# Optimization experiments

Hardware: AMD Instinct MI355X
Metric: run time of the kernel (lower is better)

The kernel has to match this reference:

```python
import jax, jax.numpy as jnp
import numpy as np

D_MODEL = 1024
D_EXPERT = 1024
NUM_EXPERTS = 8
TOP_K = 2


def setup_inputs() -> dict:
    key = jax.random.key(0)
    k_x, k_r, k1, k2, k3 = jax.random.split(key, 5)
    scale = 0.02
    x = jax.random.normal(k_x, (4, 2048, D_MODEL), dtype=jnp.float32)
    Wr = jax.random.normal(k_r, (D_MODEL, NUM_EXPERTS), dtype=jnp.float32) * scale
    # stacked per-expert SwiGLU weights (Linear with bias=False)
    W1 = jax.random.normal(k1, (NUM_EXPERTS, D_MODEL, D_EXPERT), dtype=jnp.float32) * scale
    W2 = jax.random.normal(k2, (NUM_EXPERTS, D_EXPERT, D_MODEL), dtype=jnp.float32) * scale
    W3 = jax.random.normal(k3, (NUM_EXPERTS, D_MODEL, D_EXPERT), dtype=jnp.float32) * scale
    return {"x": x, "Wr": Wr, "W1": W1, "W2": W2, "W3": W3}


def reference(x, Wr, W1, W2, W3):
    B, T, C = x.shape
    xf = x.reshape(-1, C)                       # [N, C], N = B*T
    logits = xf @ Wr                            # [N, E]
    probs = jax.nn.softmax(logits, axis=-1)
    topk_p, topk_i = jax.lax.top_k(probs, TOP_K)  # [N, K]
    topk_p = topk_p / jnp.sum(topk_p, axis=-1, keepdims=True)
    out = jnp.zeros_like(xf)
    for e in range(NUM_EXPERTS):
        # combine weight per token for this expert (0 if not routed here)
        w_e = jnp.sum(topk_p * (topk_i == e), axis=-1)  # [N]
        h = jax.nn.silu(xf @ W1[e]) * (xf @ W3[e])       # [N, d_expert]
        y = h @ W2[e]                                    # [N, C]
        out = out + w_e[:, None] * y
    return out.reshape(B, T, C)
```

## Files before the change

kernel.cpp:

```cpp
#include <hip/hip_runtime.h>
#include <hip/hip_bf16.h>

typedef __attribute__((ext_vector_type(8))) short short8;
typedef __attribute__((ext_vector_type(4))) short short4v;
typedef __attribute__((ext_vector_type(4))) unsigned short ushort4v;
typedef __attribute__((ext_vector_type(4))) float f32x4;

#define NTOK 8192
#define DM 1024
#define DE 1024
#define NE 8

__device__ __forceinline__ float bf2f(unsigned short u) {
  union { unsigned int i; float f; } v; v.i = ((unsigned int)u) << 16; return v.f;
}
__device__ __forceinline__ unsigned short f2bf(float f) {
  union { float f; unsigned int i; } v; v.f = f;
  unsigned int lsb = (v.i >> 16) & 1;
  v.i += 0x7fffu + lsb;
  return (unsigned short)(v.i >> 16);
}
__device__ __forceinline__ void gl_lds(const short* g, short* l) {
  __builtin_amdgcn_global_load_lds((const __attribute__((address_space(1))) void*)g,
                                   (__attribute__((address_space(3))) void*)l, 16, 0, 0);
}

__global__ __launch_bounds__(256) void k_transw(const float* __restrict__ W1,
                                                const float* __restrict__ W2,
                                                const float* __restrict__ W3,
                                                short* __restrict__ wcat,
                                                short* __restrict__ w2t) {
  __shared__ float t[64][65];
  int mid = blockIdx.z;
  const float* src;
  if (mid < 8)       src = W1 + (size_t)mid * (DM * DE);
  else if (mid < 16) src = W3 + (size_t)(mid - 8) * (DM * DE);
  else               src = W2 + (size_t)(mid - 16) * (DE * DM);
  int tid = threadIdx.x;
  int tr = tid >> 4, tc = tid & 15;
  int kbase = blockIdx.y * 64, nbase = blockIdx.x * 64;
#pragma unroll
  for (int j = 0; j < 4; j++) {
    int kr = tr + j * 16;
    f32x4 v = *(const f32x4*)(src + (size_t)(kbase + kr) * 1024 + nbase + tc * 4);
    t[kr][tc * 4 + 0] = v[0]; t[kr][tc * 4 + 1] = v[1];
    t[kr][tc * 4 + 2] = v[2]; t[kr][tc * 4 + 3] = v[3];
  }
  __syncthreads();
#pragma unroll
  for (int j = 0; j < 4; j++) {
    int n = tr + j * 16;
    int ng = nbase + n;
    short4v o;
    o[0] = (short)f2bf(t[tc * 4 + 0][n]);
    o[1] = (short)f2bf(t[tc * 4 + 1][n]);
    o[2] = (short)f2bf(t[tc * 4 + 2][n]);
    o[3] = (short)f2bf(t[tc * 4 + 3][n]);
    size_t dsto;
    if (mid < 16) {
      int e = mid & 7, p = mid >> 3;
      int row_out = ((ng >> 6) * 128) + p * 64 + (ng & 63);
      dsto = (size_t)e * (2048 * 1024) + (size_t)row_out * 1024 + kbase + tc * 4;
      *(short4v*)(wcat + dsto) = o;
    } else {
      int e = mid - 16;
      dsto = (size_t)e * (1024 * 1024) + (size_t)ng * 1024 + kbase + tc * 4;
      *(short4v*)(w2t + dsto) = o;
    }
  }
}

__global__ __launch_bounds__(256) void k_router(const float* __restrict__ x,
                                                const float* __restrict__ Wr,
                                                short* __restrict__ xb,
                                                int* __restrict__ esel,
                                                float* __restrict__ wgt) {
  int wid = threadIdx.x >> 6, lane = threadIdx.x & 63;
  int t = blockIdx.x * 4 + wid;
  const float* xr = x + (size_t)t * DM;
  float acc[8];
#pragma unroll
  for (int e = 0; e < 8; e++) acc[e] = 0.f;
#pragma unroll
  for (int i = 0; i < 4; i++) {
    int kb = (i * 64 + lane) * 4;
    f32x4 v = *(const f32x4*)(xr + kb);
    ushort4v ob;
#pragma unroll
    for (int j = 0; j < 4; j++) {
      f32x4 w0 = *(const f32x4*)(Wr + (size_t)(kb + j) * 8);
      f32x4 w1 = *(const f32x4*)(Wr + (size_t)(kb + j) * 8 + 4);
      float xv = v[j];
      ob[j] = f2bf(xv);
      acc[0] += xv * w0[0]; acc[1] += xv * w0[1];
      acc[2] += xv * w0[2]; acc[3] += xv * w0[3];
      acc[4] += xv * w1[0]; acc[5] += xv * w1[1];
      acc[6] += xv * w1[2]; acc[7] += xv * w1[3];
    }
    *(ushort4v*)(xb + (size_t)t * DM + kb) = ob;
  }
#pragma unroll
  for (int off = 32; off; off >>= 1)
#pragma unroll
    for (int e = 0; e < 8; e++) acc[e] += __shfl_xor(acc[e], off);
  float m0 = -1e30f, m1 = -1e30f; int e0 = 0, e1 = 0;
#pragma unroll
  for (int e = 0; e < 8; e++) {
    float v = acc[e];
    if (v > m0) { m1 = m0; e1 = e0; m0 = v; e0 = e; }
    else if (v > m1) { m1 = v; e1 = e; }
  }
  float p = __expf(m1 - m0);
  if (lane == 0) {
    esel[2 * t] = e0; esel[2 * t + 1] = e1;
    wgt[2 * t] = 1.f / (1.f + p); wgt[2 * t + 1] = p / (1.f + p);
  }
}

__global__ __launch_bounds__(256) void k_rank(const int* __restrict__ esel,
                                              int* __restrict__ cnt,
                                              int* __restrict__ rank) {
  __shared__ int wcnt[4][8];
  __shared__ int woff[4][8];
  int tid = threadIdx.x;
  int lane = tid & 63, wid = tid >> 6;
  int t = blockIdx.x * 256 + tid;
  int e0 = esel[2 * t], e1 = esel[2 * t + 1];
  unsigned long long lt = (lane == 0) ? 0ull : ((~0ull) >> (64 - lane));
  int r0 = 0, r1 = 0;
#pragma unroll
  for (int e = 0; e < 8; e++) {
    unsigned long long m0 = __ballot(e0 == e);
    unsigned long long m1 = __ballot(e1 == e);
    int c0 = __popcll(m0);
    if (e0 == e) r0 = __popcll(m0 & lt);
    if (e1 == e) r1 = c0 + __popcll(m1 & lt);
    if (lane == 0) wcnt[wid][e] = c0 + __popcll(m1);
  }
  __syncthreads();
  if (tid < 8) {
    int e = tid;
    int c0 = wcnt[0][e], c1 = wcnt[1][e], c2 = wcnt[2][e], c3 = wcnt[3][e];
    int base = atomicAdd(&cnt[e], c0 + c1 + c2 + c3);
    woff[0][e] = base;
    woff[1][e] = base + c0;
    woff[2][e] = base + c0 + c1;
    woff[3][e] = base + c0 + c1 + c2;
  }
  __syncthreads();
  rank[2 * t] = woff[wid][e0] + r0;
  rank[2 * t + 1] = woff[wid][e1] + r1;
}

__global__ void k_offsets(const int* __restrict__ cnt, int* __restrict__ off) {
  if (threadIdx.x == 0) {
    int s = 0;
    for (int e = 0; e < NE; e++) { off[e] = s; s += cnt[e]; }
  }
}

__global__ __launch_bounds__(256) void k_scatter(const int* __restrict__ off,
                                                 const int* __restrict__ esel,
                                                 const int* __restrict__ rank,
                                                 int* __restrict__ tok_of_slot,
                                                 int* __restrict__ slot_of_tok) {
  int t = blockIdx.x * 256 + threadIdx.x;
#pragma unroll
  for (int j = 0; j < 2; j++) {
    int e = esel[2 * t + j];
    int s = off[e] + rank[2 * t + j];
    tok_of_slot[s] = t;
    slot_of_tok[2 * t + j] = s;
  }
}

template<int FFN1>
__global__ __launch_bounds__(512, 4) void k_ffn(const short* __restrict__ Abase,
                                                const short* __restrict__ Bbase,
                                                const int* __restrict__ cnt,
                                                const int* __restrict__ off,
                                                const int* __restrict__ tok_of_slot,
                                                short* __restrict__ outp) {
  const int e = blockIdx.y;
  const int cnt_e = cnt[e];
  const int m0 = blockIdx.z * 256;
  if (m0 >= cnt_e) return;
  const int bse = off[e];
  const int n0 = blockIdx.x * 128;
  const short* Bt = Bbase + (size_t)e * ((FFN1 ? 2048 : 1024) * 1024) + (size_t)n0 * 1024;

  __shared__ __align__(128) short Al[3][8192];
  __shared__ __align__(128) short Bl[3][4096];

  const int tid = threadIdx.x;
  const int lane = tid & 63, wid = tid >> 6;
  const int wr = wid >> 1, wcn = wid & 1;

  const short* srcA0; const short* srcA1; const short* srcB0;
  {
    int r0 = tid >> 2, c0 = (tid & 3) ^ ((r0 >> 1) & 3);
    int row0 = m0 + r0; if (row0 >= cnt_e) row0 = cnt_e - 1;
    long ar0 = FFN1 ? (long)tok_of_slot[bse + row0] : (long)(bse + row0);
    srcA0 = Abase + ar0 * 1024 + c0 * 8;
    int ch1 = tid + 512;
    int r1 = ch1 >> 2, c1 = (ch1 & 3) ^ ((r1 >> 1) & 3);
    int row1 = m0 + r1; if (row1 >= cnt_e) row1 = cnt_e - 1;
    long ar1 = FFN1 ? (long)tok_of_slot[bse + row1] : (long)(bse + row1);
    srcA1 = Abase + ar1 * 1024 + c1 * 8;
    srcB0 = Bt + (size_t)r0 * 1024 + c0 * 8;
  }
  const int lA0 = wid * 512, lA1 = wid * 512 + 4096, lB0 = wid * 512;

  int aoff[4], boff[4];
#pragma unroll
  for (int m = 0; m < 4; m++) {
    int r = wr * 64 + m * 16 + (lane & 15);
    aoff[m] = (r * 4 + ((lane >> 4) ^ ((r >> 1) & 3))) * 16;
  }
#pragma unroll
  for (int n = 0; n < 4; n++) {
    int rb = FFN1 ? (wcn * 32 + (n & 1) * 16 + (n >> 1) * 64 + (lane & 15))
                  : (wcn * 64 + n * 16 + (lane & 15));
    boff[n] = (rb * 4 + ((lane >> 4) ^ ((rb >> 1) & 3))) * 16;
  }

  f32x4 acc[4][4];
#pragma unroll
  for (int m = 0; m < 4; m++)
#pragma unroll
    for (int n = 0; n < 4; n++) acc[m][n] = (f32x4){0.f, 0.f, 0.f, 0.f};

#define STG_A(b, kt) { gl_lds(srcA0 + (kt) * 32, &Al[b][lA0]); \
                       gl_lds(srcA1 + (kt) * 32, &Al[b][lA1]); }
#define STG_B(b, kt) { gl_lds(srcB0 + (kt) * 32, &Bl[b][lB0]); }

  STG_A(0, 0); STG_B(0, 0);
  STG_A(1, 1); STG_B(1, 1);
  asm volatile("s_waitcnt vmcnt(3)" ::: "memory");
  __builtin_amdgcn_s_barrier();

  int cur = 0, nxt = 2;
  for (int t = 0; t < 32; ++t) {
    int ktn = (t + 2 < 32) ? (t + 2) : 31;
    const char* Ab = (const char*)Al[cur];
    const char* Bb = (const char*)Bl[cur];
    short8 a[4], b[4];
#pragma unroll
    for (int m = 0; m < 4; m++) a[m] = *(const short8*)(Ab + aoff[m]);
#pragma unroll
    for (int n = 0; n < 4; n++) b[n] = *(const short8*)(Bb + boff[n]);
    STG_A(nxt, ktn); STG_B(nxt, ktn);
    __builtin_amdgcn_s_barrier();
    __builtin_amdgcn_s_setprio(1);
#pragma unroll
    for (int m = 0; m < 4; m++)
#pragma unroll
      for (int n = 0; n < 4; n++)
        acc[m][n] = __builtin_amdgcn_mfma_f32_16x16x32_bf16(a[m], b[n], acc[m][n], 0, 0, 0);
    __builtin_amdgcn_s_setprio(0);
    asm volatile("s_waitcnt vmcnt(3)" ::: "memory");
    __builtin_amdgcn_s_barrier();
    cur = (cur == 2) ? 0 : cur + 1;
    nxt = (nxt == 2) ? 0 : nxt + 1;
  }
  asm volatile("s_waitcnt vmcnt(0)" ::: "memory");

  if (FFN1) {
#pragma unroll
    for (int m = 0; m < 4; m++)
#pragma unroll
      for (int cc = 0; cc < 2; cc++) {
        f32x4 v1 = acc[m][cc], v3 = acc[m][cc + 2];
        int col = blockIdx.x * 64 + wcn * 32 + cc * 16 + (lane & 15);
#pragma unroll
        for (int i = 0; i < 4; i++) {
          int row = m0 + wr * 64 + m * 16 + ((lane >> 4) * 4) + i;
          if (row < cnt_e) {
            float a1v = v1[i];
            float hv = (a1v / (1.f + __expf(-a1v))) * v3[i];
            outp[(size_t)(bse + row) * DE + col] = (short)f2bf(hv);
          }
        }
      }
  } else {
#pragma unroll
    for (int m = 0; m < 4; m++)
#pragma unroll
      for (int n = 0; n < 4; n++) {
        f32x4 v = acc[m][n];
        int col = n0 + wcn * 64 + n * 16 + (lane & 15);
#pragma unroll
        for (int i = 0; i < 4; i++) {
          int row = m0 + wr * 64 + m * 16 + ((lane >> 4) * 4) + i;
          if (row < cnt_e)
            outp[(size_t)(bse + row) * DM + col] = (short)f2bf(v[i]);
        }
      }
  }
}

__global__ __launch_bounds__(256) void k_combine(const short* __restrict__ y,
                                                 const int* __restrict__ slot_of_tok,
                                                 const float* __restrict__ wgt,
                                                 float* __restrict__ out) {
  int t = blockIdx.x;
  int s0 = slot_of_tok[2 * t], s1 = slot_of_tok[2 * t + 1];
  float w0 = wgt[2 * t], w1 = wgt[2 * t + 1];
  int c = threadIdx.x * 4;
  short4v a = *(const short4v*)(y + (size_t)s0 * DM + c);
  short4v b = *(const short4v*)(y + (size_t)s1 * DM + c);
  f32x4 o;
#pragma unroll
  for (int j = 0; j < 4; j++)
    o[j] = w0 * bf2f((unsigned short)a[j]) + w1 * bf2f((unsigned short)b[j]);
  *(f32x4*)(out + (size_t)t * DM + c) = o;
}

extern "C" void kernel_launch(void* const* d_in, const int* in_sizes, int n_in,
                              void* d_out, int out_size, void* d_ws, size_t ws_size,
                              hipStream_t stream) {
  const float* x  = (const float*)d_in[0];
  const float* Wr = (const float*)d_in[1];
  const float* W1 = (const float*)d_in[2];
  const float* W2 = (const float*)d_in[3];
  const float* W3 = (const float*)d_in[4];
  float* out = (float*)d_out;
  char* ws = (char*)d_ws;

  short* xb   = (short*)(ws);
  short* wcat = (short*)(ws + 16777216);
  short* w2t  = (short*)(ws + 50331648);
  short* h    = (short*)(ws + 67108864);
  short* y    = (short*)(ws + 100663296);
  char* meta = ws + 134217728;
  int* cnt          = (int*)(meta);
  int* off          = (int*)(meta + 256);
  int* esel         = (int*)(meta + 512);
  int* rank         = (int*)(meta + 512 + 65536);
  int* tok_of_slot  = (int*)(meta + 512 + 2 * 65536);
  int* slot_of_tok  = (int*)(meta + 512 + 3 * 65536);
  float* wgt        = (float*)(meta + 512 + 4 * 65536);

  hipMemsetAsync(cnt, 0, 32, stream);
  k_transw<<<dim3(16, 16, 24), 256, 0, stream>>>(W1, W2, W3, wcat, w2t);
  k_router<<<2048, 256, 0, stream>>>(x, Wr, xb, esel, wgt);
  k_rank<<<32, 256, 0, stream>>>(esel, cnt, rank);
  k_offsets<<<1, 64, 0, stream>>>(cnt, off);
  k_scatter<<<32, 256, 0, stream>>>(off, esel, rank, tok_of_slot, slot_of_tok);
  k_ffn<1><<<dim3(16, 8, 32), 512, 0, stream>>>(xb, wcat, cnt, off, tok_of_slot, h);
  k_ffn<0><<<dim3(8, 8, 32), 512, 0, stream>>>(h, w2t, cnt, off, tok_of_slot, y);
  k_combine<<<8192, 256, 0, stream>>>(y, slot_of_tok, wgt, out);
}
```

Measured before the change: 244.4 us.

## Use four waves per FFN block with 128x64 per-wave tiles and drop a barrier

The grouped FFN GEMM kernels now launch 256-thread blocks instead of 512. Each of the four waves computes a 128x64 output tile with 8x4 MFMA accumulators, while the block tile stays 256x128. Each thread now issues four A and two B global-to-LDS copies per k-step, and the vmcnt waits are adjusted to match. The mid-loop barrier is removed, relying on the triple-buffered LDS ring to prevent overwrites. In exchange, fragment reuse and ILP per wave go up, but the CU has fewer resident waves to hide latency and register pressure rises.

```diff
diff --git a/kernel.cpp b/kernel.cpp
--- a/kernel.cpp
+++ b/kernel.cpp
@@ -175,7 +175,7 @@
 }
 
 template<int FFN1>
-__global__ __launch_bounds__(512, 4) void k_ffn(const short* __restrict__ Abase,
+__global__ __launch_bounds__(256, 2) void k_ffn(const short* __restrict__ Abase,
                                                 const short* __restrict__ Bbase,
                                                 const int* __restrict__ cnt,
                                                 const int* __restrict__ off,
@@ -186,8 +186,8 @@
   const int m0 = blockIdx.z * 256;
   if (m0 >= cnt_e) return;
   const int bse = off[e];
-  const int n0 = blockIdx.x * 128;
-  const short* Bt = Bbase + (size_t)e * ((FFN1 ? 2048 : 1024) * 1024) + (size_t)n0 * 1024;
+  const int nt = blockIdx.x;
+  const short* Bt = Bbase + (size_t)e * ((FFN1 ? 2048 : 1024) * 1024) + (size_t)(nt * 128) * 1024;
 
   __shared__ __align__(128) short Al[3][8192];
   __shared__ __align__(128) short Bl[3][4096];
@@ -196,25 +196,21 @@
   const int lane = tid & 63, wid = tid >> 6;
   const int wr = wid >> 1, wcn = wid & 1;
 
-  const short* srcA0; const short* srcA1; const short* srcB0;
-  {
-    int r0 = tid >> 2, c0 = (tid & 3) ^ ((r0 >> 1) & 3);
-    int row0 = m0 + r0; if (row0 >= cnt_e) row0 = cnt_e - 1;
-    long ar0 = FFN1 ? (long)tok_of_slot[bse + row0] : (long)(bse + row0);
-    srcA0 = Abase + ar0 * 1024 + c0 * 8;
-    int ch1 = tid + 512;
-    int r1 = ch1 >> 2, c1 = (ch1 & 3) ^ ((r1 >> 1) & 3);
-    int row1 = m0 + r1; if (row1 >= cnt_e) row1 = cnt_e - 1;
-    long ar1 = FFN1 ? (long)tok_of_slot[bse + row1] : (long)(bse + row1);
-    srcA1 = Abase + ar1 * 1024 + c1 * 8;
-    srcB0 = Bt + (size_t)r0 * 1024 + c0 * 8;
-  }
-  const int lA0 = wid * 512, lA1 = wid * 512 + 4096, lB0 = wid * 512;
-
-  int aoff[4], boff[4];
-#pragma unroll
-  for (int m = 0; m < 4; m++) {
-    int r = wr * 64 + m * 16 + (lane & 15);
+  const short* srcA[4]; const short* srcB[2];
+#pragma unroll
+  for (int i = 0; i < 4; i++) {
+    int ch = tid + i * 256;
+    int r = ch >> 2, c = (ch & 3) ^ ((r >> 1) & 3);
+    int row = m0 + r; if (row >= cnt_e) row = cnt_e - 1;
+    long ar = FFN1 ? (long)tok_of_slot[bse + row] : (long)(bse + row);
+    srcA[i] = Abase + ar * 1024 + c * 8;
+    if (i < 2) srcB[i] = Bt + (size_t)r * 1024 + c * 8;
+  }
+
+  int aoff[8], boff[4];
+#pragma unroll
+  for (int m = 0; m < 8; m++) {
+    int r = wr * 128 + m * 16 + (lane & 15);
     aoff[m] = (r * 4 + ((lane >> 4) ^ ((r >> 1) & 3))) * 16;
   }
 #pragma unroll
@@ -224,19 +220,22 @@
     boff[n] = (rb * 4 + ((lane >> 4) ^ ((rb >> 1) & 3))) * 16;
   }
 
-  f32x4 acc[4][4];
-#pragma unroll
-  for (int m = 0; m < 4; m++)
+  f32x4 acc[8][4];
+#pragma unroll
+  for (int m = 0; m < 8; m++)
 #pragma unroll
     for (int n = 0; n < 4; n++) acc[m][n] = (f32x4){0.f, 0.f, 0.f, 0.f};
 
-#define STG_A(b, kt) { gl_lds(srcA0 + (kt) * 32, &Al[b][lA0]); \
-                       gl_lds(srcA1 + (kt) * 32, &Al[b][lA1]); }
-#define STG_B(b, kt) { gl_lds(srcB0 + (kt) * 32, &Bl[b][lB0]); }
+#define STG_A(b, kt) { gl_lds(srcA[0] + (kt) * 32, &Al[b][(tid + 0) * 8]); \
+                       gl_lds(srcA[1] + (kt) * 32, &Al[b][(tid + 256) * 8]); \
+                       gl_lds(srcA[2] + (kt) * 32, &Al[b][(tid + 512) * 8]); \
+                       gl_lds(srcA[3] + (kt) * 32, &Al[b][(tid + 768) * 8]); }
+#define STG_B(b, kt) { gl_lds(srcB[0] + (kt) * 32, &Bl[b][(tid + 0) * 8]); \
+                       gl_lds(srcB[1] + (kt) * 32, &Bl[b][(tid + 256) * 8]); }
 
   STG_A(0, 0); STG_B(0, 0);
   STG_A(1, 1); STG_B(1, 1);
-  asm volatile("s_waitcnt vmcnt(3)" ::: "memory");
+  asm volatile("s_waitcnt vmcnt(6)" ::: "memory");
   __builtin_amdgcn_s_barrier();
 
   int cur = 0, nxt = 2;
@@ -244,21 +243,20 @@
     int ktn = (t + 2 < 32) ? (t + 2) : 31;
     const char* Ab = (const char*)Al[cur];
     const char* Bb = (const char*)Bl[cur];
-    short8 a[4], b[4];
-#pragma unroll
-    for (int m = 0; m < 4; m++) a[m] = *(const short8*)(Ab + aoff[m]);
+    short8 a[8], b[4];
+#pragma unroll
+    for (int m = 0; m < 8; m++) a[m] = *(const short8*)(Ab + aoff[m]);
 #pragma unroll
     for (int n = 0; n < 4; n++) b[n] = *(const short8*)(Bb + boff[n]);
     STG_A(nxt, ktn); STG_B(nxt, ktn);
-    __builtin_amdgcn_s_barrier();
     __builtin_amdgcn_s_setprio(1);
 #pragma unroll
-    for (int m = 0; m < 4; m++)
+    for (int m = 0; m < 8; m++)
 #pragma unroll
       for (int n = 0; n < 4; n++)
         acc[m][n] = __builtin_amdgcn_mfma_f32_16x16x32_bf16(a[m], b[n], acc[m][n], 0, 0, 0);
     __builtin_amdgcn_s_setprio(0);
-    asm volatile("s_waitcnt vmcnt(3)" ::: "memory");
+    asm volatile("s_waitcnt vmcnt(6)" ::: "memory");
     __builtin_amdgcn_s_barrier();
     cur = (cur == 2) ? 0 : cur + 1;
     nxt = (nxt == 2) ? 0 : nxt + 1;
@@ -267,14 +265,14 @@
 
   if (FFN1) {
 #pragma unroll
-    for (int m = 0; m < 4; m++)
+    for (int m = 0; m < 8; m++)
 #pragma unroll
       for (int cc = 0; cc < 2; cc++) {
         f32x4 v1 = acc[m][cc], v3 = acc[m][cc + 2];
-        int col = blockIdx.x * 64 + wcn * 32 + cc * 16 + (lane & 15);
+        int col = nt * 64 + wcn * 32 + cc * 16 + (lane & 15);
 #pragma unroll
         for (int i = 0; i < 4; i++) {
-          int row = m0 + wr * 64 + m * 16 + ((lane >> 4) * 4) + i;
+          int row = m0 + wr * 128 + m * 16 + ((lane >> 4) * 4) + i;
           if (row < cnt_e) {
             float a1v = v1[i];
             float hv = (a1v / (1.f + __expf(-a1v))) * v3[i];
@@ -284,14 +282,14 @@
       }
   } else {
 #pragma unroll
-    for (int m = 0; m < 4; m++)
+    for (int m = 0; m < 8; m++)
 #pragma unroll
       for (int n = 0; n < 4; n++) {
         f32x4 v = acc[m][n];
-        int col = n0 + wcn * 64 + n * 16 + (lane & 15);
+        int col = nt * 128 + wcn * 64 + n * 16 + (lane & 15);
 #pragma unroll
         for (int i = 0; i < 4; i++) {
-          int row = m0 + wr * 64 + m * 16 + ((lane >> 4) * 4) + i;
+          int row = m0 + wr * 128 + m * 16 + ((lane >> 4) * 4) + i;
           if (row < cnt_e)
             outp[(size_t)(bse + row) * DM + col] = (short)f2bf(v[i]);
         }
@@ -347,7 +345,7 @@
   k_rank<<<32, 256, 0, stream>>>(esel, cnt, rank);
   k_offsets<<<1, 64, 0, stream>>>(cnt, off);
   k_scatter<<<32, 256, 0, stream>>>(off, esel, rank, tok_of_slot, slot_of_tok);
-  k_ffn<1><<<dim3(16, 8, 32), 512, 0, stream>>>(xb, wcat, cnt, off, tok_of_slot, h);
-  k_ffn<0><<<dim3(8, 8, 32), 512, 0, stream>>>(h, w2t, cnt, off, tok_of_slot, y);
+  k_ffn<1><<<dim3(16, 8, 32), 256, 0, stream>>>(xb, wcat, cnt, off, tok_of_slot, h);
+  k_ffn<0><<<dim3(8, 8, 32), 256, 0, stream>>>(h, w2t, cnt, off, tok_of_slot, y);
   k_combine<<<8192, 256, 0, stream>>>(y, slot_of_tok, wgt, out);
 }
```

New measurement: 250.2 us. +2.4%, slower.
